# Optimization experiments

Measured on AMD Instinct MI355X. Metric: run time of the kernel, lower is better.

## Reference

```python
import jax, jax.numpy as jnp
import numpy as np

B, T, N, F = 4, 32, 32, 16
GH = 64            # gcn_hidden_dim
LH = 128           # lstm_hidden_dim_per_node
OUT = 1            # out_channels
LSTM_IN = GH * N   # 2048
LSTM_H = LH * N    # 4096
E = 256


def setup_inputs() -> dict:
    key = jax.random.key(0)
    ks = jax.random.split(key, 16)
    rn = lambda k, shape, s: (jax.random.normal(k, shape, dtype=jnp.float32) * s)
    inp = {}
    inp["x"] = jax.random.normal(ks[0], (B, T, N, F), dtype=jnp.float32)
    inp["edge_index"] = jax.random.randint(ks[1], (2, E), 0, N, dtype=jnp.int64)
    inp["ln_g"] = jnp.ones((F,), jnp.float32)
    inp["ln_b"] = jnp.zeros((F,), jnp.float32)
    inp["W1"] = rn(ks[2], (F, GH), 1.0 / np.sqrt(F))
    inp["b1"] = jnp.zeros((GH,), jnp.float32)
    inp["W2"] = rn(ks[3], (GH, GH), 1.0 / np.sqrt(GH))
    inp["b2"] = jnp.zeros((GH,), jnp.float32)
    s = 1.0 / np.sqrt(LSTM_H)
    inp["W_ih"] = rn(ks[4], (4 * LSTM_H, LSTM_IN), s)
    inp["b_ih"] = rn(ks[5], (4 * LSTM_H,), s)
    inp["W_hh"] = rn(ks[6], (4 * LSTM_H, LSTM_H), s)
    inp["b_hh"] = rn(ks[7], (4 * LSTM_H,), s)
    inp["fc_W"] = rn(ks[8], (OUT, LH), 1.0 / np.sqrt(LH))
    inp["fc_b"] = jnp.zeros((OUT,), jnp.float32)
    return inp


def _gcn(x, W, b, src, dst, n):
    # GCNConv: sym-normalized aggregation with self-loops, then bias.
    h = jnp.einsum('btnf,fh->btnh', x, W)                       # [B,T,N,H]
    deg = jnp.zeros((n,), h.dtype).at[dst].add(1.0)
    dinv = jnp.where(deg > 0, jax.lax.rsqrt(jnp.maximum(deg, 1.0)), 0.0)
    coef = (dinv[src] * dinv[dst]).astype(h.dtype)              # [E+N]
    msgs = h[:, :, src, :] * coef[None, None, :, None]          # gather
    agg = jnp.zeros_like(h).at[:, :, dst, :].add(msgs)          # scatter-add
    return agg + b


def _layernorm(x, g, b, eps=1e-5):
    mu = jnp.mean(x, axis=-1, keepdims=True)
    var = jnp.mean(jnp.square(x - mu), axis=-1, keepdims=True)
    return (x - mu) * jax.lax.rsqrt(var + eps) * g + b


def _lstm_last(seq, W_ih, b_ih, W_hh, b_hh):
    # seq: [B,T,D]; returns last hidden state [B,H]
    Bs = seq.shape[0]
    H = W_hh.shape[1]
    x_proj = jnp.einsum('btd,gd->btg', seq, W_ih) + b_ih + b_hh  # [B,T,4H]

    def step(carry, xg):
        h, c = carry
        gates = xg + h @ W_hh.T
        i, f, g, o = jnp.split(gates, 4, axis=-1)
        c = jax.nn.sigmoid(f) * c + jax.nn.sigmoid(i) * jnp.tanh(g)
        h = jax.nn.sigmoid(o) * jnp.tanh(c)
        return (h, c), None

    h0 = jnp.zeros((Bs, H), seq.dtype)
    (h_last, _), _ = jax.lax.scan(step, (h0, h0), jnp.swapaxes(x_proj, 0, 1))
    return h_last


def reference(x, edge_index, ln_g, ln_b, W1, b1, W2, b2, W_ih, b_ih, W_hh, b_hh, fc_W, fc_b):
    n = N
    loops = jnp.arange(n, dtype=edge_index.dtype)
    src = jnp.concatenate([edge_index[0], loops])
    dst = jnp.concatenate([edge_index[1], loops])

    h = _layernorm(x, ln_g, ln_b)
    h = _gcn(h, W1, b1, src, dst, n)
    h = _gcn(h, W2, b2, src, dst, n)
    b, t, nn_, f = h.shape
    h = h.reshape(b, t, nn_ * f)                                # [B,T,N*GH]
    h = _lstm_last(h, W_ih, b_ih, W_hh, b_hh)                   # [B,N*LH]
    h = h.reshape(b, nn_, -1)                                   # [B,N,LH]
    return h @ fc_W.T + fc_b                                    # [B,N,OUT]
```

## Files before the change

kernel.cpp:

```cpp
#include <hip/hip_runtime.h>
#include <math.h>

#define T_STEPS 32
#define NNODES  32
#define FEAT    16
#define GHID    64
#define LSTM_IN 2048
#define LSTM_H  4096
#define GATES   16384
#define BT      128

typedef __attribute__((ext_vector_type(8))) short bhalf8;
typedef __attribute__((ext_vector_type(4))) float floatx4;

__device__ __forceinline__ float sigmoidf_(float x) { return 1.0f / (1.0f + __expf(-x)); }

__device__ __forceinline__ unsigned short f2bf(float f) {
    unsigned int u = __float_as_uint(f);
    u += 0x7FFFu + ((u >> 16) & 1u);
    return (unsigned short)(u >> 16);
}
__device__ __forceinline__ float bf_lo(unsigned int u) { return __uint_as_float(u << 16); }
__device__ __forceinline__ float bf_hi(unsigned int u) { return __uint_as_float(u & 0xFFFF0000u); }

__global__ void zero_f(float* p, int n) {
    int i = blockIdx.x * 256 + threadIdx.x;
    if (i < n) p[i] = 0.0f;
}

__global__ void conv_bf16(const float* __restrict__ src, unsigned short* __restrict__ dst, int n4) {
    int i = blockIdx.x * 256 + threadIdx.x;
    if (i < n4) {
        float4 v = ((const float4*)src)[i];
        ushort4 o;
        o.x = f2bf(v.x); o.y = f2bf(v.y); o.z = f2bf(v.z); o.w = f2bf(v.w);
        ((ushort4*)dst)[i] = o;
    }
}

__global__ void build_adj(const int* __restrict__ ei, int E, float* __restrict__ A) {
    __shared__ float As[NNODES * NNODES];
    __shared__ int   deg[NNODES];
    __shared__ float dinv[NNODES];
    int tid = threadIdx.x;
    if (tid < NNODES) deg[tid] = 1;
    for (int i = tid; i < NNODES * NNODES; i += 256) As[i] = 0.0f;
    __syncthreads();
    for (int e = tid; e < E; e += 256) atomicAdd(&deg[ei[E + e]], 1);
    __syncthreads();
    if (tid < NNODES) dinv[tid] = rsqrtf((float)deg[tid]);
    __syncthreads();
    for (int e = tid; e < E; e += 256) {
        int s = ei[e], d = ei[E + e];
        atomicAdd(&As[d * NNODES + s], dinv[s] * dinv[d]);
    }
    if (tid < NNODES) atomicAdd(&As[tid * NNODES + tid], dinv[tid] * dinv[tid]);
    __syncthreads();
    for (int i = tid; i < NNODES * NNODES; i += 256) A[i] = As[i];
}

__global__ __launch_bounds__(256) void gcn2_kernel(
    const float* __restrict__ x, const float* __restrict__ ln_g, const float* __restrict__ ln_b,
    const float* __restrict__ W1, const float* __restrict__ b1,
    const float* __restrict__ W2, const float* __restrict__ b2,
    const float* __restrict__ A, float* __restrict__ seq)
{
    __shared__ float As[NNODES * NNODES];
    __shared__ float w1[FEAT * GHID];
    __shared__ float w2[GHID * GHID];
    __shared__ float xln[NNODES * FEAT];
    __shared__ float h1[NNODES * GHID];
    __shared__ float g1[NNODES * GHID];
    __shared__ float h2[NNODES * GHID];

    int tid = threadIdx.x;
    int bt = blockIdx.x;
    const float* xb = x + (size_t)bt * NNODES * FEAT;

    for (int i = tid; i < 1024; i += 256) As[i] = A[i];
    for (int i = tid; i < FEAT * GHID; i += 256) w1[i] = W1[i];
    for (int i = tid; i < GHID * GHID; i += 256) w2[i] = W2[i];
    for (int i = tid; i < NNODES * FEAT; i += 256) xln[i] = xb[i];
    __syncthreads();

    if (tid < NNODES) {
        float mu = 0.0f;
        for (int f = 0; f < FEAT; ++f) mu += xln[tid * FEAT + f];
        mu *= (1.0f / FEAT);
        float var = 0.0f;
        for (int f = 0; f < FEAT; ++f) { float d = xln[tid * FEAT + f] - mu; var += d * d; }
        var *= (1.0f / FEAT);
        float r = rsqrtf(var + 1e-5f);
        for (int f = 0; f < FEAT; ++f)
            xln[tid * FEAT + f] = (xln[tid * FEAT + f] - mu) * r * ln_g[f] + ln_b[f];
    }
    __syncthreads();

    for (int idx = tid; idx < NNODES * GHID; idx += 256) {
        int n = idx >> 6, j = idx & 63;
        float s = 0.0f;
        #pragma unroll
        for (int f = 0; f < FEAT; ++f) s += xln[n * FEAT + f] * w1[f * GHID + j];
        h1[idx] = s;
    }
    __syncthreads();
    for (int idx = tid; idx < NNODES * GHID; idx += 256) {
        int n = idx >> 6, j = idx & 63;
        float s = b1[j];
        #pragma unroll 8
        for (int m = 0; m < NNODES; ++m) s += As[n * NNODES + m] * h1[m * GHID + j];
        g1[idx] = s;
    }
    __syncthreads();
    for (int idx = tid; idx < NNODES * GHID; idx += 256) {
        int n = idx >> 6, j = idx & 63;
        float s = 0.0f;
        #pragma unroll 8
        for (int k = 0; k < GHID; ++k) s += g1[n * GHID + k] * w2[k * GHID + j];
        h2[idx] = s;
    }
    __syncthreads();
    for (int idx = tid; idx < NNODES * GHID; idx += 256) {
        int n = idx >> 6, j = idx & 63;
        float s = b2[j];
        #pragma unroll 8
        for (int m = 0; m < NNODES; ++m) s += As[n * NNODES + m] * h2[m * GHID + j];
        seq[(size_t)bt * LSTM_IN + idx] = s;
    }
}

__global__ __launch_bounds__(256) void xproj_mfma(
    const float* __restrict__ seq, const float* __restrict__ W_ih,
    float* __restrict__ xpart)
{
    int lane = threadIdx.x & 63;
    int wid = blockIdx.x * 4 + (threadIdx.x >> 6);
    int ntile = wid >> 2;
    int kc = wid & 3;
    int n0 = ntile << 4;
    int rr = lane & 15;
    int kg = lane >> 4;

    floatx4 acc[8];
    #pragma unroll
    for (int mt = 0; mt < 8; ++mt) acc[mt] = (floatx4){0.f, 0.f, 0.f, 0.f};

    for (int ks = 0; ks < 16; ++ks) {
        int k0 = (kc << 9) + (ks << 5) + (kg << 3);
        const float4* wp = (const float4*)(W_ih + (size_t)(n0 + rr) * LSTM_IN + k0);
        float4 w0 = wp[0], w1 = wp[1];
        bhalf8 bf;
        bf[0] = (short)f2bf(w0.x); bf[1] = (short)f2bf(w0.y);
        bf[2] = (short)f2bf(w0.z); bf[3] = (short)f2bf(w0.w);
        bf[4] = (short)f2bf(w1.x); bf[5] = (short)f2bf(w1.y);
        bf[6] = (short)f2bf(w1.z); bf[7] = (short)f2bf(w1.w);
        #pragma unroll
        for (int mt = 0; mt < 8; ++mt) {
            const float4* ap = (const float4*)(seq + (size_t)(mt * 16 + rr) * LSTM_IN + k0);
            float4 a0 = ap[0], a1 = ap[1];
            bhalf8 af;
            af[0] = (short)f2bf(a0.x); af[1] = (short)f2bf(a0.y);
            af[2] = (short)f2bf(a0.z); af[3] = (short)f2bf(a0.w);
            af[4] = (short)f2bf(a1.x); af[5] = (short)f2bf(a1.y);
            af[6] = (short)f2bf(a1.z); af[7] = (short)f2bf(a1.w);
            acc[mt] = __builtin_amdgcn_mfma_f32_16x16x32_bf16(af, bf, acc[mt], 0, 0, 0);
        }
    }
    float* xo = xpart + (size_t)kc * (BT * GATES);
    #pragma unroll
    for (int mt = 0; mt < 8; ++mt) {
        #pragma unroll
        for (int i = 0; i < 4; ++i) {
            int row = mt * 16 + kg * 4 + i;
            xo[(size_t)row * GATES + n0 + rr] = acc[mt][i];
        }
    }
}

__global__ void combine_xp(const float* __restrict__ xpart,
                           const float* __restrict__ b_ih, const float* __restrict__ b_hh,
                           float* __restrict__ xp)
{
    int i = blockIdx.x * 256 + threadIdx.x;
    const float4* p0 = (const float4*)xpart;
    const float4* p1 = p0 + (BT * GATES / 4);
    const float4* p2 = p1 + (BT * GATES / 4);
    const float4* p3 = p2 + (BT * GATES / 4);
    float4 a = p0[i], b = p1[i], c = p2[i], d = p3[i];
    int col = (i & (GATES / 4 - 1)) << 2;
    float4 o;
    o.x = a.x + b.x + c.x + d.x + b_ih[col + 0] + b_hh[col + 0];
    o.y = a.y + b.y + c.y + d.y + b_ih[col + 1] + b_hh[col + 1];
    o.z = a.z + b.z + c.z + d.z + b_ih[col + 2] + b_hh[col + 2];
    o.w = a.w + b.w + c.w + d.w + b_ih[col + 3] + b_hh[col + 3];
    ((float4*)xp)[i] = o;
}

__global__ __launch_bounds__(256) void lstm_step_bf16(
    const unsigned short* __restrict__ Wbf, const float* __restrict__ xp,
    const unsigned short* __restrict__ hin, unsigned short* __restrict__ hout,
    float* __restrict__ hf32, float* __restrict__ c, int t)
{
    int lane = threadIdx.x & 63;
    int w = threadIdx.x >> 6;
    int j = blockIdx.x * 4 + w;

    float acc[4][4];
    #pragma unroll
    for (int g = 0; g < 4; ++g)
        #pragma unroll
        for (int b = 0; b < 4; ++b) acc[g][b] = 0.0f;

    #pragma unroll 1
    for (int ks = 0; ks < 8; ++ks) {
        int kb = ks * 512 + lane * 8;
        float h8[4][8];
        #pragma unroll
        for (int b = 0; b < 4; ++b) {
            uint4 hv = *(const uint4*)(hin + b * LSTM_H + kb);
            h8[b][0] = bf_lo(hv.x); h8[b][1] = bf_hi(hv.x);
            h8[b][2] = bf_lo(hv.y); h8[b][3] = bf_hi(hv.y);
            h8[b][4] = bf_lo(hv.z); h8[b][5] = bf_hi(hv.z);
            h8[b][6] = bf_lo(hv.w); h8[b][7] = bf_hi(hv.w);
        }
        #pragma unroll
        for (int g = 0; g < 4; ++g) {
            uint4 wv = *(const uint4*)(Wbf + ((size_t)(g * LSTM_H + j) << 12) + kb);
            float w8[8];
            w8[0] = bf_lo(wv.x); w8[1] = bf_hi(wv.x);
            w8[2] = bf_lo(wv.y); w8[3] = bf_hi(wv.y);
            w8[4] = bf_lo(wv.z); w8[5] = bf_hi(wv.z);
            w8[6] = bf_lo(wv.w); w8[7] = bf_hi(wv.w);
            #pragma unroll
            for (int k = 0; k < 8; ++k) {
                acc[g][0] += w8[k] * h8[0][k];
                acc[g][1] += w8[k] * h8[1][k];
                acc[g][2] += w8[k] * h8[2][k];
                acc[g][3] += w8[k] * h8[3][k];
            }
        }
    }

    #pragma unroll
    for (int off = 32; off > 0; off >>= 1) {
        #pragma unroll
        for (int g = 0; g < 4; ++g)
            #pragma unroll
            for (int b = 0; b < 4; ++b)
                acc[g][b] += __shfl_xor(acc[g][b], off, 64);
    }

    if (lane < 4) {
        int b = lane;
        size_t xb = ((size_t)(b * T_STEPS + t)) * GATES + j;
        float gi = sigmoidf_(acc[0][b] + xp[xb]);
        float gf = sigmoidf_(acc[1][b] + xp[xb + LSTM_H]);
        float gg = tanhf   (acc[2][b] + xp[xb + 2 * LSTM_H]);
        float go = sigmoidf_(acc[3][b] + xp[xb + 3 * LSTM_H]);
        float cn = gf * c[b * LSTM_H + j] + gi * gg;
        float hn = go * tanhf(cn);
        c[b * LSTM_H + j] = cn;
        hf32[b * LSTM_H + j] = hn;
        hout[b * LSTM_H + j] = f2bf(hn);
    }
}

__global__ void final_fc(const float* __restrict__ h, const float* __restrict__ fcW,
                         const float* __restrict__ fcb, float* __restrict__ out)
{
    int i = threadIdx.x;
    if (i < 128) {
        int b = i >> 5, n = i & 31;
        const float* hp = h + (size_t)b * LSTM_H + n * 128;
        float s = 0.0f;
        #pragma unroll 8
        for (int l = 0; l < 128; ++l) s += hp[l] * fcW[l];
        out[i] = s + fcb[0];
    }
}

extern "C" void kernel_launch(void* const* d_in, const int* in_sizes, int n_in,
                              void* d_out, int out_size, void* d_ws, size_t ws_size,
                              hipStream_t stream)
{
    const float* x    = (const float*)d_in[0];
    const int*   ei   = (const int*)d_in[1];
    const float* ln_g = (const float*)d_in[2];
    const float* ln_b = (const float*)d_in[3];
    const float* W1   = (const float*)d_in[4];
    const float* b1   = (const float*)d_in[5];
    const float* W2   = (const float*)d_in[6];
    const float* b2   = (const float*)d_in[7];
    const float* W_ih = (const float*)d_in[8];
    const float* b_ih = (const float*)d_in[9];
    const float* W_hh = (const float*)d_in[10];
    const float* b_hh = (const float*)d_in[11];
    const float* fcW  = (const float*)d_in[12];
    const float* fcb  = (const float*)d_in[13];
    int E = in_sizes[1] / 2;

    float* ws    = (float*)d_ws;
    float* A     = ws;
    float* seq   = A + 1024;
    float* xp    = seq + 262144;
    float* xpart = xp + 2097152;
    float* c     = xpart + 8388608;
    float* hbf0f = c + 16384;
    float* hbf1f = hbf0f + 8192;
    float* hf32  = hbf1f + 8192;
    float* WbfF  = hf32 + 16384;
    unsigned short* hbf0 = (unsigned short*)hbf0f;
    unsigned short* hbf1 = (unsigned short*)hbf1f;
    unsigned short* Wbf  = (unsigned short*)WbfF;

    zero_f<<<dim3(96), dim3(256), 0, stream>>>(c, 24576);
    build_adj<<<dim3(1), dim3(256), 0, stream>>>(ei, E, A);
    gcn2_kernel<<<dim3(BT), dim3(256), 0, stream>>>(x, ln_g, ln_b, W1, b1, W2, b2, A, seq);
    conv_bf16<<<dim3(65536), dim3(256), 0, stream>>>(W_hh, Wbf, GATES * LSTM_H / 4);
    xproj_mfma<<<dim3(1024), dim3(256), 0, stream>>>(seq, W_ih, xpart);
    combine_xp<<<dim3(2048), dim3(256), 0, stream>>>(xpart, b_ih, b_hh, xp);

    for (int t = 0; t < T_STEPS; ++t) {
        const unsigned short* hin = (t & 1) ? hbf1 : hbf0;
        unsigned short* hout      = (t & 1) ? hbf0 : hbf1;
        lstm_step_bf16<<<dim3(LSTM_H / 4), dim3(256), 0, stream>>>(Wbf, xp, hin, hout, hf32, c, t);
    }
    final_fc<<<dim3(1), dim3(128), 0, stream>>>(hf32, fcW, fcb, (float*)d_out);
}
```

Measured before the change: 1.354 ms.

## Replace per-step LSTM launches with persistent cooperative kernel holding W_hh in registers

Swaps the 32 per-timestep LSTM launches for one cooperative persistent kernel of 256 blocks that converts its slice of W_hh to bf16 once and keeps it in registers across all steps. Each step uses MFMA 16x16x32 bf16 instructions, reduces partial sums in shared memory, keeps the cell state in a register and synchronises with grid.sync. This removes the separate fp32-to-bf16 weight conversion pass and the re-reading of W_hh on every step. In exchange it depends on cooperative launch co-residency (256 blocks of 1024 threads with about 128 registers of weights each) and pays one grid-wide barrier per step.

```diff
diff --git a/kernel.cpp b/kernel.cpp
--- a/kernel.cpp
+++ b/kernel.cpp
@@ -1,5 +1,8 @@
 #include <hip/hip_runtime.h>
+#include <hip/hip_cooperative_groups.h>
 #include <math.h>
+
+namespace cg = cooperative_groups;
 
 #define T_STEPS 32
 #define NNODES  32
@@ -19,23 +22,6 @@
     unsigned int u = __float_as_uint(f);
     u += 0x7FFFu + ((u >> 16) & 1u);
     return (unsigned short)(u >> 16);
-}
-__device__ __forceinline__ float bf_lo(unsigned int u) { return __uint_as_float(u << 16); }
-__device__ __forceinline__ float bf_hi(unsigned int u) { return __uint_as_float(u & 0xFFFF0000u); }
-
-__global__ void zero_f(float* p, int n) {
-    int i = blockIdx.x * 256 + threadIdx.x;
-    if (i < n) p[i] = 0.0f;
-}
-
-__global__ void conv_bf16(const float* __restrict__ src, unsigned short* __restrict__ dst, int n4) {
-    int i = blockIdx.x * 256 + threadIdx.x;
-    if (i < n4) {
-        float4 v = ((const float4*)src)[i];
-        ushort4 o;
-        o.x = f2bf(v.x); o.y = f2bf(v.y); o.z = f2bf(v.z); o.w = f2bf(v.w);
-        ((ushort4*)dst)[i] = o;
-    }
 }
 
 __global__ void build_adj(const int* __restrict__ ei, int E, float* __restrict__ A) {
@@ -196,72 +182,99 @@
     ((float4*)xp)[i] = o;
 }
 
-__global__ __launch_bounds__(256) void lstm_step_bf16(
-    const unsigned short* __restrict__ Wbf, const float* __restrict__ xp,
-    const unsigned short* __restrict__ hin, unsigned short* __restrict__ hout,
-    float* __restrict__ hf32, float* __restrict__ c, int t)
-{
-    int lane = threadIdx.x & 63;
-    int w = threadIdx.x >> 6;
-    int j = blockIdx.x * 4 + w;
-
-    float acc[4][4];
+__global__ __launch_bounds__(1024, 4) void lstm_persistent(
+    const float* __restrict__ W_hh, const float* __restrict__ xp,
+    unsigned short* __restrict__ h0, unsigned short* __restrict__ h1,
+    float* __restrict__ hf32)
+{
+    __shared__ floatx4 part[16 * 64];
+    __shared__ float gv[4][4][16];
+
+    const int tid   = threadIdx.x;
+    const int lane  = tid & 63;
+    const int wv    = tid >> 6;
+    const int bid   = blockIdx.x;
+    const int rr    = lane & 15;
+    const int kg    = lane >> 4;
+    const int g     = wv >> 2;
+    const int kp    = wv & 3;
+    const int jbase = bid << 4;
+    const int kbase = kp << 10;
+
+    const float* wrow = W_hh + (size_t)(g * LSTM_H + jbase + rr) * LSTM_H + kbase + (kg << 3);
+    bhalf8 wfrag[32];
     #pragma unroll
-    for (int g = 0; g < 4; ++g)
+    for (int ks = 0; ks < 32; ++ks) {
+        const float4* wp = (const float4*)(wrow + ks * 32);
+        float4 a = wp[0], b = wp[1];
+        bhalf8 w;
+        w[0] = (short)f2bf(a.x); w[1] = (short)f2bf(a.y);
+        w[2] = (short)f2bf(a.z); w[3] = (short)f2bf(a.w);
+        w[4] = (short)f2bf(b.x); w[5] = (short)f2bf(b.y);
+        w[6] = (short)f2bf(b.z); w[7] = (short)f2bf(b.w);
+        wfrag[ks] = w;
+    }
+
+    if (tid < 64) h0[(bid << 6) + tid] = 0;
+
+    float creg = 0.0f;
+
+    cg::grid_group grid = cg::this_grid();
+    grid.sync();
+
+    const int arow = (rr & 3) * LSTM_H + kbase + (kg << 3);
+
+    for (int t = 0; t < T_STEPS; ++t) {
+        const unsigned short* hc = (t & 1) ? h1 : h0;
+        unsigned short* hn       = (t & 1) ? h0 : h1;
+
+        float xpv0 = 0.f, xpv1 = 0.f, xpv2 = 0.f, xpv3 = 0.f;
+        size_t xb = 0;
+        if (wv == 0) {
+            xb = ((size_t)(kg * T_STEPS + t)) * GATES + jbase + rr;
+            xpv0 = xp[xb];
+            xpv1 = xp[xb + LSTM_H];
+            xpv2 = xp[xb + 2 * LSTM_H];
+            xpv3 = xp[xb + 3 * LSTM_H];
+        }
+
+        floatx4 acc = (floatx4){0.f, 0.f, 0.f, 0.f};
         #pragma unroll
-        for (int b = 0; b < 4; ++b) acc[g][b] = 0.0f;
-
-    #pragma unroll 1
-    for (int ks = 0; ks < 8; ++ks) {
-        int kb = ks * 512 + lane * 8;
-        float h8[4][8];
-        #pragma unroll
-        for (int b = 0; b < 4; ++b) {
-            uint4 hv = *(const uint4*)(hin + b * LSTM_H + kb);
-            h8[b][0] = bf_lo(hv.x); h8[b][1] = bf_hi(hv.x);
-            h8[b][2] = bf_lo(hv.y); h8[b][3] = bf_hi(hv.y);
-            h8[b][4] = bf_lo(hv.z); h8[b][5] = bf_hi(hv.z);
-            h8[b][6] = bf_lo(hv.w); h8[b][7] = bf_hi(hv.w);
-        }
-        #pragma unroll
-        for (int g = 0; g < 4; ++g) {
-            uint4 wv = *(const uint4*)(Wbf + ((size_t)(g * LSTM_H + j) << 12) + kb);
-            float w8[8];
-            w8[0] = bf_lo(wv.x); w8[1] = bf_hi(wv.x);
-            w8[2] = bf_lo(wv.y); w8[3] = bf_hi(wv.y);
-            w8[4] = bf_lo(wv.z); w8[5] = bf_hi(wv.z);
-            w8[6] = bf_lo(wv.w); w8[7] = bf_hi(wv.w);
-            #pragma unroll
-            for (int k = 0; k < 8; ++k) {
-                acc[g][0] += w8[k] * h8[0][k];
-                acc[g][1] += w8[k] * h8[1][k];
-                acc[g][2] += w8[k] * h8[2][k];
-                acc[g][3] += w8[k] * h8[3][k];
+        for (int ks = 0; ks < 32; ++ks) {
+            bhalf8 af = *(const bhalf8*)(hc + arow + ks * 32);
+            acc = __builtin_amdgcn_mfma_f32_16x16x32_bf16(af, wfrag[ks], acc, 0, 0, 0);
+        }
+        part[wv * 64 + lane] = acc;
+        __syncthreads();
+
+        if (wv < 4) {
+            floatx4 r0 = part[(wv * 4 + 0) * 64 + lane];
+            floatx4 r1 = part[(wv * 4 + 1) * 64 + lane];
+            floatx4 r2 = part[(wv * 4 + 2) * 64 + lane];
+            floatx4 r3 = part[(wv * 4 + 3) * 64 + lane];
+            floatx4 r = (r0 + r1) + (r2 + r3);
+            if (kg == 0) {
+                #pragma unroll
+                for (int i = 0; i < 4; ++i) gv[wv][i][rr] = r[i];
             }
         }
-    }
-
-    #pragma unroll
-    for (int off = 32; off > 0; off >>= 1) {
-        #pragma unroll
-        for (int g = 0; g < 4; ++g)
-            #pragma unroll
-            for (int b = 0; b < 4; ++b)
-                acc[g][b] += __shfl_xor(acc[g][b], off, 64);
-    }
-
-    if (lane < 4) {
-        int b = lane;
-        size_t xb = ((size_t)(b * T_STEPS + t)) * GATES + j;
-        float gi = sigmoidf_(acc[0][b] + xp[xb]);
-        float gf = sigmoidf_(acc[1][b] + xp[xb + LSTM_H]);
-        float gg = tanhf   (acc[2][b] + xp[xb + 2 * LSTM_H]);
-        float go = sigmoidf_(acc[3][b] + xp[xb + 3 * LSTM_H]);
-        float cn = gf * c[b * LSTM_H + j] + gi * gg;
-        float hn = go * tanhf(cn);
-        c[b * LSTM_H + j] = cn;
-        hf32[b * LSTM_H + j] = hn;
-        hout[b * LSTM_H + j] = f2bf(hn);
+        __syncthreads();
+
+        if (wv == 0) {
+            const int batch = kg;
+            const int col   = rr;
+            float gi = sigmoidf_(gv[0][batch][col] + xpv0);
+            float gf = sigmoidf_(gv[1][batch][col] + xpv1);
+            float gg = tanhf   (gv[2][batch][col] + xpv2);
+            float go = sigmoidf_(gv[3][batch][col] + xpv3);
+            float cn = gf * creg + gi * gg;
+            float hv = go * tanhf(cn);
+            creg = cn;
+            hn[batch * LSTM_H + jbase + col] = f2bf(hv);
+            if (t == T_STEPS - 1) hf32[batch * LSTM_H + jbase + col] = hv;
+        }
+        __threadfence();
+        grid.sync();
     }
 }
 
@@ -304,26 +317,22 @@
     float* seq   = A + 1024;
     float* xp    = seq + 262144;
     float* xpart = xp + 2097152;
-    float* c     = xpart + 8388608;
-    float* hbf0f = c + 16384;
-    float* hbf1f = hbf0f + 8192;
-    float* hf32  = hbf1f + 8192;
-    float* WbfF  = hf32 + 16384;
-    unsigned short* hbf0 = (unsigned short*)hbf0f;
-    unsigned short* hbf1 = (unsigned short*)hbf1f;
-    unsigned short* Wbf  = (unsigned short*)WbfF;
-
-    zero_f<<<dim3(96), dim3(256), 0, stream>>>(c, 24576);
+    float* hf32  = xpart + 8388608;
+    unsigned short* hb0 = (unsigned short*)(hf32 + 16384);
+    unsigned short* hb1 = (unsigned short*)(hf32 + 16384 + 8192);
+
     build_adj<<<dim3(1), dim3(256), 0, stream>>>(ei, E, A);
     gcn2_kernel<<<dim3(BT), dim3(256), 0, stream>>>(x, ln_g, ln_b, W1, b1, W2, b2, A, seq);
-    conv_bf16<<<dim3(65536), dim3(256), 0, stream>>>(W_hh, Wbf, GATES * LSTM_H / 4);
     xproj_mfma<<<dim3(1024), dim3(256), 0, stream>>>(seq, W_ih, xpart);
     combine_xp<<<dim3(2048), dim3(256), 0, stream>>>(xpart, b_ih, b_hh, xp);
 
-    for (int t = 0; t < T_STEPS; ++t) {
-        const unsigned short* hin = (t & 1) ? hbf1 : hbf0;
-        unsigned short* hout      = (t & 1) ? hbf0 : hbf1;
-        lstm_step_bf16<<<dim3(LSTM_H / 4), dim3(256), 0, stream>>>(Wbf, xp, hin, hout, hf32, c, t);
-    }
+    void* kargs[5];
+    kargs[0] = (void*)&W_hh;
+    kargs[1] = (void*)&xp;
+    kargs[2] = (void*)&hb0;
+    kargs[3] = (void*)&hb1;
+    kargs[4] = (void*)&hf32;
+    hipLaunchCooperativeKernel(lstm_persistent, dim3(256), dim3(1024), kargs, 0, stream);
+
     final_fc<<<dim3(1), dim3(128), 0, stream>>>(hf32, fcW, fcb, (float*)d_out);
 }
```

Result: slower. 4.216 ms (+211.2%).
